# Kernel tuning notes

Hardware: AMD Instinct MI355X
Metric: run time of the kernel (lower is better)

Reference implementation:

```python
import jax, jax.numpy as jnp
import numpy as np

SEQ, BATCH, IN, H = 188, 256, 128, 256


def _lstm_scan(x_proj, w_hh, batch, hidden):
    # x_proj: (T, B, 4H) = input projection + biases, already computed
    h0 = jnp.zeros((batch, hidden), x_proj.dtype)
    c0 = jnp.zeros((batch, hidden), x_proj.dtype)
    w_hh_t = w_hh.T  # (H, 4H)

    def step(carry, xt):
        h, c = carry
        gates = xt + h @ w_hh_t  # (B, 4H)
        i, f, g, o = jnp.split(gates, 4, axis=-1)  # PyTorch gate order i,f,g,o
        i = jax.nn.sigmoid(i)
        f = jax.nn.sigmoid(f)
        g = jnp.tanh(g)
        o = jax.nn.sigmoid(o)
        c = f * c + i * g
        h = o * jnp.tanh(c)
        return (h, c), h

    _, hs = jax.lax.scan(step, (h0, c0), x_proj)
    return hs  # (T, B, H)


def setup_inputs() -> dict:
    key = jax.random.key(0)
    ks = jax.random.split(key, 9)
    s = 1.0 / np.sqrt(H)  # PyTorch default init scale
    mk = lambda k, shape: jax.random.uniform(k, shape, jnp.float32, -s, s)
    return {
        "x": jax.random.normal(ks[0], (SEQ, BATCH, IN), jnp.float32),
        "w_ih_f": mk(ks[1], (4 * H, IN)),
        "w_hh_f": mk(ks[2], (4 * H, H)),
        "b_ih_f": mk(ks[3], (4 * H,)),
        "b_hh_f": mk(ks[4], (4 * H,)),
        "w_ih_b": mk(ks[5], (4 * H, IN)),
        "w_hh_b": mk(ks[6], (4 * H, H)),
        "b_ih_b": mk(ks[7], (4 * H,)),
        "b_hh_b": mk(ks[8], (4 * H,)),
    }


def reference(x, w_ih_f, w_hh_f, b_ih_f, b_hh_f, w_ih_b, w_hh_b, b_ih_b, b_hh_b):
    batch = x.shape[1]
    # Precompute input projections for all timesteps (big GEMM outside the scan)
    xp_f = jnp.einsum('tbi,gi->tbg', x, w_ih_f) + b_ih_f + b_hh_f
    xp_b = jnp.einsum('tbi,gi->tbg', x[::-1], w_ih_b) + b_ih_b + b_hh_b
    out_f = _lstm_scan(xp_f, w_hh_f, batch, H)            # (T, B, H)
    out_b = _lstm_scan(xp_b, w_hh_b, batch, H)[::-1]      # reversed back
    return jnp.concatenate([out_f, out_b], axis=-1)       # (T, B, 2H)
```

## Files before the change

kernel.cpp:

```cpp
#include <hip/hip_runtime.h>

#define T_SEQ 188
#define NB    256
#define NIN   128
#define NH    256
#define SCQ   (0.0625f / 16129.0f)

typedef __attribute__((ext_vector_type(8))) short s16x8;
typedef __attribute__((ext_vector_type(4))) short s16x4;
typedef __attribute__((ext_vector_type(4))) float f32x4;
typedef __attribute__((ext_vector_type(4))) int   i32x4;

__device__ __forceinline__ short f2bf(float f) {
    union { float f; unsigned u; } v; v.f = f;
    unsigned r = v.u + 0x7fffu + ((v.u >> 16) & 1u);
    return (short)(r >> 16);
}
__device__ __forceinline__ float bf2f(unsigned short s) {
    union { unsigned u; float f; } t; t.u = ((unsigned)s) << 16; return t.f;
}
__device__ __forceinline__ float sigf(float x) {
    return __builtin_amdgcn_rcpf(1.0f + __expf(-x));
}
__device__ __forceinline__ float tanh_(float x) {
    return 1.0f - 2.0f * __builtin_amdgcn_rcpf(__expf(2.0f * x) + 1.0f);
}

__device__ __forceinline__ void lds_barrier() {
    asm volatile("s_waitcnt lgkmcnt(0)" ::: "memory");
    __builtin_amdgcn_s_barrier();
    asm volatile("" ::: "memory");
}

__global__ __launch_bounds__(256) void xp_gemm(
    const float* __restrict__ x,
    const float* __restrict__ w_ih_f, const float* __restrict__ w_ih_b,
    const float* __restrict__ b_ih_f, const float* __restrict__ b_hh_f,
    const float* __restrict__ b_ih_b, const float* __restrict__ b_hh_b,
    unsigned short* __restrict__ xp)
{
    const int mt = blockIdx.x >> 5;
    const int dn = blockIdx.x & 31;
    const int d  = dn >> 4, nt = dn & 15;
    const int t  = mt >> 2, b0 = (mt & 3) * 64, Nb = nt * 64;
    const float* w_ih = d ? w_ih_b : w_ih_f;
    const float* b_ih = d ? b_ih_b : b_ih_f;
    const float* b_hh = d ? b_hh_b : b_hh_f;
    const int tid = threadIdx.x;

    __shared__ short xl[64][136];
    __shared__ short wl[64][136];

    #pragma unroll
    for (int j = 0; j < 8; ++j) {
        const int c2 = tid + j * 256;
        const int r = c2 >> 5, o4 = (c2 & 31) * 4;
        float4 xv = *(const float4*)(x + ((size_t)(t * NB + b0 + r)) * NIN + o4);
        s16x4 xs; xs[0] = f2bf(xv.x); xs[1] = f2bf(xv.y); xs[2] = f2bf(xv.z); xs[3] = f2bf(xv.w);
        *(s16x4*)&xl[r][o4] = xs;
        float4 wv = *(const float4*)(w_ih + ((size_t)(Nb + r)) * NIN + o4);
        s16x4 ws_; ws_[0] = f2bf(wv.x); ws_[1] = f2bf(wv.y); ws_[2] = f2bf(wv.z); ws_[3] = f2bf(wv.w);
        *(s16x4*)&wl[r][o4] = ws_;
    }
    __syncthreads();

    const int v = tid >> 6, l = tid & 63, lg = l >> 4, lb = l & 15;
    s16x8 a[4];
    #pragma unroll
    for (int kk = 0; kk < 4; ++kk)
        a[kk] = *(const s16x8*)&xl[16 * v + lb][kk * 32 + 8 * lg];
    f32x4 acc[4];
    #pragma unroll
    for (int nf = 0; nf < 4; ++nf) {
        const int g = Nb + nf * 16 + lb;
        const float bs = b_ih[g] + b_hh[g];
        acc[nf][0] = bs; acc[nf][1] = bs; acc[nf][2] = bs; acc[nf][3] = bs;
    }
    #pragma unroll
    for (int kk = 0; kk < 4; ++kk)
        #pragma unroll
        for (int nf = 0; nf < 4; ++nf) {
            s16x8 bf_ = *(const s16x8*)&wl[nf * 16 + lb][kk * 32 + 8 * lg];
            acc[nf] = __builtin_amdgcn_mfma_f32_16x16x32_bf16(a[kk], bf_, acc[nf], 0, 0, 0);
        }
    #pragma unroll
    for (int nf = 0; nf < 4; ++nf)
        #pragma unroll
        for (int rr = 0; rr < 4; ++rr) {
            const int b = b0 + 16 * v + 4 * lg + rr;
            xp[((size_t)(d * T_SEQ + t) * NB + b) * 1024 + Nb + nf * 16 + lb] =
                (unsigned short)f2bf(acc[nf][rr]);
        }
}

__device__ __forceinline__ void lstm_step(
    int p, int w, int l, int lg, int lb, int c, int huq, int hwb,
    const unsigned short*& xpp, long dxp, float*& outp, long dout,
    int* hl, int (&rscr)[16][4][4][16],
    const i32x4 (&wq)[4][4], float& cst,
    unsigned short (&cur)[4], unsigned short (&nxt)[4])
{
    #pragma unroll
    for (int G = 0; G < 4; ++G)
        nxt[G] = xpp[G * 256];
    xpp += dxp;

    i32x4 ac[4];
    #pragma unroll
    for (int G = 0; G < 4; ++G) {
        ac[G][0] = 0; ac[G][1] = 0; ac[G][2] = 0; ac[G][3] = 0;
    }
    #pragma unroll
    for (int kk = 0; kk < 4; ++kk) {
        i32x4 bq = *(const i32x4*)&hl[p * 1024 + kk * 256 + 4 * l];
        ac[0] = __builtin_amdgcn_mfma_i32_16x16x64_i8(wq[0][kk], bq, ac[0], 0, 0, 0);
        ac[1] = __builtin_amdgcn_mfma_i32_16x16x64_i8(wq[1][kk], bq, ac[1], 0, 0, 0);
        ac[2] = __builtin_amdgcn_mfma_i32_16x16x64_i8(wq[2][kk], bq, ac[2], 0, 0, 0);
        ac[3] = __builtin_amdgcn_mfma_i32_16x16x64_i8(wq[3][kk], bq, ac[3], 0, 0, 0);
    }

    if (lb < 4) {
        #pragma unroll
        for (int G = 0; G < 4; ++G)
            *(i32x4*)&rscr[w][G][lb][4 * lg] = ac[G];
    }
    asm volatile("s_waitcnt lgkmcnt(0)" ::: "memory");
    int av[4];
    #pragma unroll
    for (int G = 0; G < 4; ++G)
        av[G] = rscr[w][G][c][huq];
    asm volatile("s_waitcnt lgkmcnt(0)" ::: "memory");

    const float gi = SCQ * (float)av[0] + bf2f(cur[0]);
    const float gf = SCQ * (float)av[1] + bf2f(cur[1]);
    const float gg = SCQ * (float)av[2] + bf2f(cur[2]);
    const float go = SCQ * (float)av[3] + bf2f(cur[3]);
    const float iv = sigf(gi), fv = sigf(gf);
    const float gv = tanh_(gg), ov = sigf(go);
    const float cc = fv * cst + iv * gv;
    cst = cc;
    const float h = ov * tanh_(cc);
    *outp = h;
    outp += dout;
    ((signed char*)hl)[(p ^ 1) * 4096 + hwb] = (signed char)(int)rintf(h * 127.0f);

    lds_barrier();
}

__global__ __launch_bounds__(1024, 4) void lstm_rec(
    const float* __restrict__ w_hh_f, const float* __restrict__ w_hh_b,
    const unsigned short* __restrict__ xp, float* __restrict__ out)
{
    const int bid = blockIdx.x;
    const int d  = bid >> 6;
    const int bt = bid & 63;
    const float* w_hh = d ? w_hh_b : w_hh_f;
    const int tid = threadIdx.x;
    const int w = tid >> 6, l = tid & 63, lg = l >> 4, lb = l & 15;
    const int c = l & 3, huq = l >> 2;

    __shared__ int hl[2 * 1024];
    __shared__ int rscr[16][4][4][16];

    i32x4 wq[4][4];
    #pragma unroll
    for (int G = 0; G < 4; ++G) {
        const int row = G * 256 + 16 * w + lb;
        #pragma unroll
        for (int kk = 0; kk < 4; ++kk) {
            i32x4 pk;
            #pragma unroll
            for (int r = 0; r < 4; ++r) {
                float4 wv = *(const float4*)(w_hh + (size_t)row * NH + kk * 64 + 16 * lg + 4 * r);
                const int q0 = (int)rintf(wv.x * 2032.0f) & 255;
                const int q1 = (int)rintf(wv.y * 2032.0f) & 255;
                const int q2 = (int)rintf(wv.z * 2032.0f) & 255;
                const int q3 = (int)rintf(wv.w * 2032.0f) & 255;
                pk[r] = q0 | (q1 << 8) | (q2 << 16) | (q3 << 24);
            }
            wq[G][kk] = pk;
        }
    }
    for (int i = tid; i < 2048; i += 1024) hl[i] = 0;

    const int hwb = (w >> 2) * 1024 + (w & 3) * 256 + c * 16 + huq;

    float cst = 0.f;
    unsigned short XPA[4], XPB[4];
    const int t0 = d ? (T_SEQ - 1) : 0;
    const long dxp  = (d ? -(long)NB : (long)NB) * 1024;
    const long dout = (d ? -(long)NB : (long)NB) * 512;
    const unsigned short* xpp =
        xp + ((size_t)(d * T_SEQ + t0) * NB + bt * 4 + c) * 1024 + 16 * w + huq;
    float* outp = out + ((size_t)t0 * NB + bt * 4 + c) * 512 + d * 256 + 16 * w + huq;
    #pragma unroll
    for (int G = 0; G < 4; ++G)
        XPA[G] = xpp[G * 256];
    xpp += dxp;
    __syncthreads();

    for (int s2 = 0; s2 < T_SEQ / 2; ++s2) {
        lstm_step(0, w, l, lg, lb, c, huq, hwb, xpp, dxp, outp, dout,
                  hl, rscr, wq, cst, XPA, XPB);
        lstm_step(1, w, l, lg, lb, c, huq, hwb, xpp, dxp, outp, dout,
                  hl, rscr, wq, cst, XPB, XPA);
    }
}

#define ZSTR_FB 392
__global__ __launch_bounds__(512, 2) void lstm_fb(
    const float* __restrict__ x,
    const float* __restrict__ w_ih_f, const float* __restrict__ w_hh_f,
    const float* __restrict__ b_ih_f, const float* __restrict__ b_hh_f,
    const float* __restrict__ w_ih_b, const float* __restrict__ w_hh_b,
    const float* __restrict__ b_ih_b, const float* __restrict__ b_hh_b,
    float* __restrict__ out, unsigned* __restrict__ flags)
{
    const int b  = blockIdx.x;
    const int d  = b >> 5;
    const int hh = (b >> 4) & 1;
    const int bt = b & 15;
    const int pb = b ^ 16;
    const int po = 1 - hh;
    const float* w_ih = d ? w_ih_b : w_ih_f;
    const float* w_hh = d ? w_hh_b : w_hh_f;
    const float* b_ih = d ? b_ih_b : b_ih_f;
    const float* b_hh = d ? b_hh_b : b_hh_f;
    const int tid = threadIdx.x;
    const int w = tid >> 6, l = tid & 63, lg = l >> 4, lb = l & 15;
    const int hbase = hh * 128 + 16 * w;

    __shared__ short Z[2][16][ZSTR_FB];
    __shared__ float biasL[8][4][16];
    const int off_x   = lg * 8;
    const int off_own = (4 + 4 * hh) * 32 + lg * 8;
    const int off_par = (4 + 4 * po) * 32 + lg * 8;

    s16x8 wf[4][12];
    #pragma unroll
    for (int G = 0; G < 4; ++G) {
        const int gc = G * 256 + hbase + lb;
        #pragma unroll
        for (int kkidx = 0; kkidx < 12; ++kkidx) {
            const int kb = (kkidx < 4) ? (off_x + 32 * kkidx)
                         : (kkidx < 8) ? (off_own + 32 * (kkidx - 4))
                                       : (off_par + 32 * (kkidx - 8));
            const float* src = (kb < NIN) ? (w_ih + (size_t)gc * NIN + kb)
                                          : (w_hh + (size_t)gc * NH + (kb - NIN));
            float4 a  = *(const float4*)(src);
            float4 b2 = *(const float4*)(src + 4);
            s16x8 tv;
            tv[0] = f2bf(a.x);  tv[1] = f2bf(a.y);  tv[2] = f2bf(a.z);  tv[3] = f2bf(a.w);
            tv[4] = f2bf(b2.x); tv[5] = f2bf(b2.y); tv[6] = f2bf(b2.z); tv[7] = f2bf(b2.w);
            wf[G][kkidx] = tv;
        }
    }
    {
        const int G = lb >> 2, r = lb & 3;
        const int gcr = G * 256 + hbase + 4 * lg + r;
        biasL[w][G][4 * lg + r] = b_ih[gcr] + b_hh[gcr];
    }
    const int srow = tid >> 5;
    const int sk4  = (tid & 31) * 4;
    {
        s16x8 zz;
        #pragma unroll
        for (int i = 0; i < 8; ++i) zz[i] = 0;
        *(s16x8*)&Z[0][srow][NIN + (tid & 31) * 8] = zz;
        const int t0 = d ? (T_SEQ - 1) : 0;
        float4 xv0 = *(const float4*)(x + ((size_t)(t0 * NB + bt * 16 + srow)) * NIN + sk4);
        s16x4 xp_;
        xp_[0] = f2bf(xv0.x); xp_[1] = f2bf(xv0.y); xp_[2] = f2bf(xv0.z); xp_[3] = f2bf(xv0.w);
        *(s16x4*)&Z[0][srow][sk4] = xp_;
    }
    float cst[4] = {0.f, 0.f, 0.f, 0.f};
    __syncthreads();
    unsigned* myflag = flags + b * 16;
    unsigned* pflag  = flags + pb * 16;
    float* outp = out + (size_t)(bt * 16) * 512 + d * 256 + hbase + 4 * lg;

    for (int s = 0; s < T_SEQ; ++s) {
        const int p = s & 1;
        const int t = d ? (T_SEQ - 1 - s) : s;
        float4 xv;
        const bool havex = (s + 1 < T_SEQ);
        if (havex) {
            const int tn = d ? (T_SEQ - 2 - s) : (s + 1);
            xv = *(const float4*)(x + ((size_t)(tn * NB + bt * 16 + srow)) * NIN + sk4);
        }
        f32x4 acc[4];
        #pragma unroll
        for (int G = 0; G < 4; ++G)
            acc[G] = *(const f32x4*)&biasL[w][G][4 * lg];
        const short* zrow = &Z[p][lb][0];
        #pragma unroll
        for (int kk = 0; kk < 4; ++kk) {
            s16x8 bfv = *(const s16x8*)(zrow + off_x + 32 * kk);
            acc[0] = __builtin_amdgcn_mfma_f32_16x16x32_bf16(wf[0][kk], bfv, acc[0], 0, 0, 0);
            acc[1] = __builtin_amdgcn_mfma_f32_16x16x32_bf16(wf[1][kk], bfv, acc[1], 0, 0, 0);
            acc[2] = __builtin_amdgcn_mfma_f32_16x16x32_bf16(wf[2][kk], bfv, acc[2], 0, 0, 0);
            acc[3] = __builtin_amdgcn_mfma_f32_16x16x32_bf16(wf[3][kk], bfv, acc[3], 0, 0, 0);
        }
        #pragma unroll
        for (int kk = 0; kk < 4; ++kk) {
            s16x8 bfv = *(const s16x8*)(zrow + off_own + 32 * kk);
            acc[0] = __builtin_amdgcn_mfma_f32_16x16x32_bf16(wf[0][4 + kk], bfv, acc[0], 0, 0, 0);
            acc[1] = __builtin_amdgcn_mfma_f32_16x16x32_bf16(wf[1][4 + kk], bfv, acc[1], 0, 0, 0);
            acc[2] = __builtin_amdgcn_mfma_f32_16x16x32_bf16(wf[2][4 + kk], bfv, acc[2], 0, 0, 0);
            acc[3] = __builtin_amdgcn_mfma_f32_16x16x32_bf16(wf[3][4 + kk], bfv, acc[3], 0, 0, 0);
        }
        if (s > 0) {
            const unsigned want = (unsigned)s;
            while (__hip_atomic_load(pflag, __ATOMIC_RELAXED, __HIP_MEMORY_SCOPE_AGENT) < want)
                __builtin_amdgcn_s_sleep(1);
            __builtin_amdgcn_fence(__ATOMIC_ACQUIRE, "agent");
            const int tprev = d ? (T_SEQ - s) : (s - 1);
            float4 pv = *(const float4*)(out + (size_t)tprev * NB * 512
                         + (size_t)(bt * 16 + srow) * 512 + d * 256 + po * 128 + sk4);
            s16x4 pp;
            pp[0] = f2bf(pv.x); pp[1] = f2bf(pv.y); pp[2] = f2bf(pv.z); pp[3] = f2bf(pv.w);
            *(s16x4*)&Z[p][srow][NIN + po * 128 + sk4] = pp;
        }
        __syncthreads();
        #pragma unroll
        for (int kk = 0; kk < 4; ++kk) {
            s16x8 bfv = *(const s16x8*)(zrow + off_par + 32 * kk);
            acc[0] = __builtin_amdgcn_mfma_f32_16x16x32_bf16(wf[0][8 + kk], bfv, acc[0], 0, 0, 0);
            acc[1] = __builtin_amdgcn_mfma_f32_16x16x32_bf16(wf[1][8 + kk], bfv, acc[1], 0, 0, 0);
            acc[2] = __builtin_amdgcn_mfma_f32_16x16x32_bf16(wf[2][8 + kk], bfv, acc[2], 0, 0, 0);
            acc[3] = __builtin_amdgcn_mfma_f32_16x16x32_bf16(wf[3][8 + kk], bfv, acc[3], 0, 0, 0);
        }
        float4 hout; s16x4 hbf;
        #pragma unroll
        for (int r = 0; r < 4; ++r) {
            const float iv = sigf(acc[0][r]);
            const float fv = sigf(acc[1][r]);
            const float gv = tanh_(acc[2][r]);
            const float ov = sigf(acc[3][r]);
            const float cc = fv * cst[r] + iv * gv;
            cst[r] = cc;
            const float h = ov * tanh_(cc);
            (&hout.x)[r] = h;
            hbf[r] = f2bf(h);
        }
        *(s16x4*)&Z[p ^ 1][lb][NIN + hbase + 4 * lg] = hbf;
        if (havex) {
            s16x4 xp_;
            xp_[0] = f2bf(xv.x); xp_[1] = f2bf(xv.y); xp_[2] = f2bf(xv.z); xp_[3] = f2bf(xv.w);
            *(s16x4*)&Z[p ^ 1][srow][sk4] = xp_;
        }
        *(f32x4*)(outp + (size_t)t * NB * 512 + lb * 512) = *(f32x4*)&hout;
        __syncthreads();
        if (tid == 0 && s + 1 < T_SEQ)
            __hip_atomic_store(myflag, (unsigned)(s + 1),
                               __ATOMIC_RELEASE, __HIP_MEMORY_SCOPE_AGENT);
    }
}

extern "C" void kernel_launch(void* const* d_in, const int* in_sizes, int n_in,
                              void* d_out, int out_size, void* d_ws, size_t ws_size,
                              hipStream_t stream) {
    const float* x      = (const float*)d_in[0];
    const float* w_ih_f = (const float*)d_in[1];
    const float* w_hh_f = (const float*)d_in[2];
    const float* b_ih_f = (const float*)d_in[3];
    const float* b_hh_f = (const float*)d_in[4];
    const float* w_ih_b = (const float*)d_in[5];
    const float* w_hh_b = (const float*)d_in[6];
    const float* b_ih_b = (const float*)d_in[7];
    const float* b_hh_b = (const float*)d_in[8];
    float* out = (float*)d_out;

    const size_t XPN = (size_t)2 * T_SEQ * NB * 1024;
    const int g1 = (T_SEQ * NB / 64) * 32;

    if (ws_size >= XPN * 2) {
        unsigned short* xp = (unsigned short*)d_ws;
        xp_gemm<<<dim3(g1), dim3(256), 0, stream>>>(
            x, w_ih_f, w_ih_b, b_ih_f, b_hh_f, b_ih_b, b_hh_b, xp);
        lstm_rec<<<dim3(128), dim3(1024), 0, stream>>>(w_hh_f, w_hh_b, xp, out);
    } else {
        unsigned* flags = (unsigned*)d_ws;
        hipMemsetAsync(flags, 0, 4096, stream);
        lstm_fb<<<dim3(64), dim3(512), 0, stream>>>(
            x, w_ih_f, w_hh_f, b_ih_f, b_hh_f, w_ih_b, w_hh_b, b_ih_b, b_hh_b,
            out, flags);
    }
}
```

Before: 349.4 us.

## Split batch columns into two groups and overlap MFMA with gate math

Restructures the recurrent LSTM kernel so the four batch columns per block form two groups whose hidden states live in separate LDS buffers. In each half-step, all waves run the int8 MFMA for one group while the waves owning the other group compute their gate nonlinearities, interleaving matrix and elementwise work across the serial time dependency. It removes the ping-pong h buffers and the per-step x-projection double buffering. It adds a second barrier per timestep and leaves half the waves idle during each gates phase.

```diff
diff --git a/kernel.cpp b/kernel.cpp
--- a/kernel.cpp
+++ b/kernel.cpp
@@ -93,48 +93,43 @@
         }
 }
 
-__device__ __forceinline__ void lstm_step(
-    int p, int w, int l, int lg, int lb, int c, int huq, int hwb,
-    const unsigned short*& xpp, long dxp, float*& outp, long dout,
-    int* hl, int (&rscr)[16][4][4][16],
-    const i32x4 (&wq)[4][4], float& cst,
-    unsigned short (&cur)[4], unsigned short (&nxt)[4])
-{
-    #pragma unroll
-    for (int G = 0; G < 4; ++G)
-        nxt[G] = xpp[G * 256];
-    xpp += dxp;
-
+__device__ __forceinline__ void mfma_phase(
+    const int* buf, int (*rs)[256], int cb,
+    int w, int l, int lg, int lb, const i32x4 (&wq)[4][4])
+{
     i32x4 ac[4];
     #pragma unroll
-    for (int G = 0; G < 4; ++G) {
-        ac[G][0] = 0; ac[G][1] = 0; ac[G][2] = 0; ac[G][3] = 0;
-    }
+    for (int G = 0; G < 4; ++G) { ac[G][0] = 0; ac[G][1] = 0; ac[G][2] = 0; ac[G][3] = 0; }
     #pragma unroll
     for (int kk = 0; kk < 4; ++kk) {
-        i32x4 bq = *(const i32x4*)&hl[p * 1024 + kk * 256 + 4 * l];
+        i32x4 bq = *(const i32x4*)&buf[kk * 256 + 4 * l];
         ac[0] = __builtin_amdgcn_mfma_i32_16x16x64_i8(wq[0][kk], bq, ac[0], 0, 0, 0);
         ac[1] = __builtin_amdgcn_mfma_i32_16x16x64_i8(wq[1][kk], bq, ac[1], 0, 0, 0);
         ac[2] = __builtin_amdgcn_mfma_i32_16x16x64_i8(wq[2][kk], bq, ac[2], 0, 0, 0);
         ac[3] = __builtin_amdgcn_mfma_i32_16x16x64_i8(wq[3][kk], bq, ac[3], 0, 0, 0);
     }
-
-    if (lb < 4) {
+    if (lb >= cb && lb < cb + 2) {
+        const int c1 = lb - cb;
         #pragma unroll
         for (int G = 0; G < 4; ++G)
-            *(i32x4*)&rscr[w][G][lb][4 * lg] = ac[G];
-    }
-    asm volatile("s_waitcnt lgkmcnt(0)" ::: "memory");
-    int av[4];
-    #pragma unroll
-    for (int G = 0; G < 4; ++G)
-        av[G] = rscr[w][G][c][huq];
-    asm volatile("s_waitcnt lgkmcnt(0)" ::: "memory");
-
-    const float gi = SCQ * (float)av[0] + bf2f(cur[0]);
-    const float gf = SCQ * (float)av[1] + bf2f(cur[1]);
-    const float gg = SCQ * (float)av[2] + bf2f(cur[2]);
-    const float go = SCQ * (float)av[3] + bf2f(cur[3]);
+            *(i32x4*)&rs[G * 2 + c1][16 * w + 4 * lg] = ac[G];
+    }
+}
+
+__device__ __forceinline__ void gates_phase(
+    const int (*rs)[256], int lq, int hu,
+    float& cst, unsigned short (&X)[4],
+    const unsigned short*& xpp, long dxp, float*& outp, long dout,
+    signed char* hlbyte)
+{
+    const int a0 = rs[0 + lq][hu];
+    const int a1 = rs[2 + lq][hu];
+    const int a2 = rs[4 + lq][hu];
+    const int a3 = rs[6 + lq][hu];
+    const float gi = SCQ * (float)a0 + bf2f(X[0]);
+    const float gf = SCQ * (float)a1 + bf2f(X[1]);
+    const float gg = SCQ * (float)a2 + bf2f(X[2]);
+    const float go = SCQ * (float)a3 + bf2f(X[3]);
     const float iv = sigf(gi), fv = sigf(gf);
     const float gv = tanh_(gg), ov = sigf(go);
     const float cc = fv * cst + iv * gv;
@@ -142,9 +137,9 @@
     const float h = ov * tanh_(cc);
     *outp = h;
     outp += dout;
-    ((signed char*)hl)[(p ^ 1) * 4096 + hwb] = (signed char)(int)rintf(h * 127.0f);
-
-    lds_barrier();
+    *hlbyte = (signed char)(int)rintf(h * 127.0f);
+    X[0] = xpp[0]; X[1] = xpp[256]; X[2] = xpp[512]; X[3] = xpp[768];
+    xpp += dxp;
 }
 
 __global__ __launch_bounds__(1024, 4) void lstm_rec(
@@ -157,10 +152,14 @@
     const float* w_hh = d ? w_hh_b : w_hh_f;
     const int tid = threadIdx.x;
     const int w = tid >> 6, l = tid & 63, lg = l >> 4, lb = l & 15;
-    const int c = l & 3, huq = l >> 2;
-
-    __shared__ int hl[2 * 1024];
-    __shared__ int rscr[16][4][4][16];
+    const int grp = w >> 3;
+    const int gw  = w & 7;
+    const int lq  = l & 1;
+    const int hu  = 32 * gw + (l >> 1);
+    const int c   = 2 * grp + lq;
+
+    __shared__ int hlA[1024], hlB[1024];
+    __shared__ int rsA[8][256], rsB[8][256];
 
     i32x4 wq[4][4];
     #pragma unroll
@@ -181,29 +180,36 @@
             wq[G][kk] = pk;
         }
     }
-    for (int i = tid; i < 2048; i += 1024) hl[i] = 0;
-
-    const int hwb = (w >> 2) * 1024 + (w & 3) * 256 + c * 16 + huq;
+    hlA[tid] = 0; hlB[tid] = 0;
+
+    const int hlw = (hu >> 6) * 1024 + ((hu >> 4) & 3) * 256 + c * 16 + (hu & 15);
+    signed char* hlbyte = (signed char*)(grp ? hlB : hlA) + hlw;
 
     float cst = 0.f;
-    unsigned short XPA[4], XPB[4];
+    unsigned short X[4];
     const int t0 = d ? (T_SEQ - 1) : 0;
     const long dxp  = (d ? -(long)NB : (long)NB) * 1024;
     const long dout = (d ? -(long)NB : (long)NB) * 512;
     const unsigned short* xpp =
-        xp + ((size_t)(d * T_SEQ + t0) * NB + bt * 4 + c) * 1024 + 16 * w + huq;
-    float* outp = out + ((size_t)t0 * NB + bt * 4 + c) * 512 + d * 256 + 16 * w + huq;
-    #pragma unroll
-    for (int G = 0; G < 4; ++G)
-        XPA[G] = xpp[G * 256];
+        xp + ((size_t)(d * T_SEQ + t0) * NB + bt * 4 + c) * 1024 + hu;
+    float* outp = out + ((size_t)t0 * NB + bt * 4 + c) * 512 + d * 256 + hu;
+    X[0] = xpp[0]; X[1] = xpp[256]; X[2] = xpp[512]; X[3] = xpp[768];
     xpp += dxp;
     __syncthreads();
 
-    for (int s2 = 0; s2 < T_SEQ / 2; ++s2) {
-        lstm_step(0, w, l, lg, lb, c, huq, hwb, xpp, dxp, outp, dout,
-                  hl, rscr, wq, cst, XPA, XPB);
-        lstm_step(1, w, l, lg, lb, c, huq, hwb, xpp, dxp, outp, dout,
-                  hl, rscr, wq, cst, XPB, XPA);
+    mfma_phase(hlA, rsA, 0, w, l, lg, lb, wq);
+    lds_barrier();
+
+    for (int s = 0; s < T_SEQ; ++s) {
+        mfma_phase(hlB, rsB, 2, w, l, lg, lb, wq);
+        if (grp == 0)
+            gates_phase(rsA, lq, hu, cst, X, xpp, dxp, outp, dout, hlbyte);
+        lds_barrier();
+        if (s < T_SEQ - 1)
+            mfma_phase(hlA, rsA, 0, w, l, lg, lb, wq);
+        if (grp == 1)
+            gates_phase(rsB, lq, hu, cst, X, xpp, dxp, outp, dout, hlbyte);
+        lds_barrier();
     }
 }
 
```

After: 475.9 us. 1.36x slower.

## Restructure input-projection GEMM to loop over N tiles with resident A fragments

Applied to the files above, without the earlier changes.

The xp_gemm kernel now launches one block per (64-row M tile, direction) and loops over all 16 N tiles, keeping the converted x fragments in registers instead of reloading and reconverting x for every N tile. Biases are pre-summed once into LDS, and each N-tile iteration stages its weight slice through LDS with two barriers. This cuts redundant x loads and conversions and shrinks the grid, at the cost of serializing 16 tiles per block with extra barriers and less parallelism. The recurrent kernel's hidden-index arithmetic is rewritten equivalently.

```diff
diff --git a/kernel.cpp b/kernel.cpp
--- a/kernel.cpp
+++ b/kernel.cpp
@@ -39,58 +39,86 @@
     const float* __restrict__ b_ih_b, const float* __restrict__ b_hh_b,
     unsigned short* __restrict__ xp)
 {
-    const int mt = blockIdx.x >> 5;
-    const int dn = blockIdx.x & 31;
-    const int d  = dn >> 4, nt = dn & 15;
-    const int t  = mt >> 2, b0 = (mt & 3) * 64, Nb = nt * 64;
+    const int mt = blockIdx.x >> 1;
+    const int d  = blockIdx.x & 1;
+    const int t  = mt >> 2, b0 = (mt & 3) * 64;
     const float* w_ih = d ? w_ih_b : w_ih_f;
     const float* b_ih = d ? b_ih_b : b_ih_f;
     const float* b_hh = d ? b_hh_b : b_hh_f;
     const int tid = threadIdx.x;
-
-    __shared__ short xl[64][136];
+    const int v = tid >> 6, l = tid & 63, lg = l >> 4, lb = l & 15;
+
     __shared__ short wl[64][136];
-
-    #pragma unroll
-    for (int j = 0; j < 8; ++j) {
-        const int c2 = tid + j * 256;
-        const int r = c2 >> 5, o4 = (c2 & 31) * 4;
-        float4 xv = *(const float4*)(x + ((size_t)(t * NB + b0 + r)) * NIN + o4);
-        s16x4 xs; xs[0] = f2bf(xv.x); xs[1] = f2bf(xv.y); xs[2] = f2bf(xv.z); xs[3] = f2bf(xv.w);
-        *(s16x4*)&xl[r][o4] = xs;
-        float4 wv = *(const float4*)(w_ih + ((size_t)(Nb + r)) * NIN + o4);
-        s16x4 ws_; ws_[0] = f2bf(wv.x); ws_[1] = f2bf(wv.y); ws_[2] = f2bf(wv.z); ws_[3] = f2bf(wv.w);
-        *(s16x4*)&wl[r][o4] = ws_;
-    }
-    __syncthreads();
-
-    const int v = tid >> 6, l = tid & 63, lg = l >> 4, lb = l & 15;
+    __shared__ float biasS[1024];
+
+    #pragma unroll
+    for (int j = 0; j < 4; ++j) {
+        const int g = tid * 4 + j * 1024; (void)g;
+    }
+    {
+        const int g = tid * 4;
+        float4 bi = *(const float4*)(b_ih + g);
+        float4 bh = *(const float4*)(b_hh + g);
+        biasS[g + 0] = bi.x + bh.x; biasS[g + 1] = bi.y + bh.y;
+        biasS[g + 2] = bi.z + bh.z; biasS[g + 3] = bi.w + bh.w;
+    }
+
     s16x8 a[4];
-    #pragma unroll
-    for (int kk = 0; kk < 4; ++kk)
-        a[kk] = *(const s16x8*)&xl[16 * v + lb][kk * 32 + 8 * lg];
-    f32x4 acc[4];
-    #pragma unroll
-    for (int nf = 0; nf < 4; ++nf) {
-        const int g = Nb + nf * 16 + lb;
-        const float bs = b_ih[g] + b_hh[g];
-        acc[nf][0] = bs; acc[nf][1] = bs; acc[nf][2] = bs; acc[nf][3] = bs;
-    }
-    #pragma unroll
-    for (int kk = 0; kk < 4; ++kk)
+    {
+        const float* xr = x + ((size_t)(t * NB + b0 + 16 * v + lb)) * NIN + 8 * lg;
+        #pragma unroll
+        for (int kk = 0; kk < 4; ++kk) {
+            float4 p0 = *(const float4*)(xr + 32 * kk);
+            float4 p1 = *(const float4*)(xr + 32 * kk + 4);
+            s16x8 tv;
+            tv[0] = f2bf(p0.x); tv[1] = f2bf(p0.y); tv[2] = f2bf(p0.z); tv[3] = f2bf(p0.w);
+            tv[4] = f2bf(p1.x); tv[5] = f2bf(p1.y); tv[6] = f2bf(p1.z); tv[7] = f2bf(p1.w);
+            a[kk] = tv;
+        }
+    }
+
+    const int wr = tid >> 2, wk = (tid & 3) * 32;
+
+    unsigned short* xpb =
+        xp + ((size_t)(d * T_SEQ + t) * NB + b0 + 16 * v + 4 * lg) * 1024 + lb;
+
+    for (int nt = 0; nt < 16; ++nt) {
+        const int Nb = nt * 64;
+        {
+            const float* wsrc = w_ih + ((size_t)(Nb + wr)) * NIN + wk;
+            #pragma unroll
+            for (int j = 0; j < 4; ++j) {
+                float4 p0 = *(const float4*)(wsrc + 8 * j);
+                float4 p1 = *(const float4*)(wsrc + 8 * j + 4);
+                s16x8 tv;
+                tv[0] = f2bf(p0.x); tv[1] = f2bf(p0.y); tv[2] = f2bf(p0.z); tv[3] = f2bf(p0.w);
+                tv[4] = f2bf(p1.x); tv[5] = f2bf(p1.y); tv[6] = f2bf(p1.z); tv[7] = f2bf(p1.w);
+                *(s16x8*)&wl[wr][wk + 8 * j] = tv;
+            }
+        }
+        __syncthreads();
+
+        f32x4 acc[4];
         #pragma unroll
         for (int nf = 0; nf < 4; ++nf) {
-            s16x8 bf_ = *(const s16x8*)&wl[nf * 16 + lb][kk * 32 + 8 * lg];
-            acc[nf] = __builtin_amdgcn_mfma_f32_16x16x32_bf16(a[kk], bf_, acc[nf], 0, 0, 0);
-        }
-    #pragma unroll
-    for (int nf = 0; nf < 4; ++nf)
-        #pragma unroll
-        for (int rr = 0; rr < 4; ++rr) {
-            const int b = b0 + 16 * v + 4 * lg + rr;
-            xp[((size_t)(d * T_SEQ + t) * NB + b) * 1024 + Nb + nf * 16 + lb] =
-                (unsigned short)f2bf(acc[nf][rr]);
-        }
+            const float bs = biasS[Nb + nf * 16 + lb];
+            acc[nf][0] = bs; acc[nf][1] = bs; acc[nf][2] = bs; acc[nf][3] = bs;
+        }
+        #pragma unroll
+        for (int kk = 0; kk < 4; ++kk)
+            #pragma unroll
+            for (int nf = 0; nf < 4; ++nf) {
+                s16x8 bf_ = *(const s16x8*)&wl[nf * 16 + lb][kk * 32 + 8 * lg];
+                acc[nf] = __builtin_amdgcn_mfma_f32_16x16x32_bf16(a[kk], bf_, acc[nf], 0, 0, 0);
+            }
+        __syncthreads();
+
+        #pragma unroll
+        for (int nf = 0; nf < 4; ++nf)
+            #pragma unroll
+            for (int rr = 0; rr < 4; ++rr)
+                xpb[(size_t)rr * 1024 + Nb + nf * 16] = (unsigned short)f2bf(acc[nf][rr]);
+    }
 }
 
 __device__ __forceinline__ void lstm_step(
@@ -183,7 +211,8 @@
     }
     for (int i = tid; i < 2048; i += 1024) hl[i] = 0;
 
-    const int hwb = (w >> 2) * 1024 + (w & 3) * 256 + c * 16 + huq;
+    const int hu = 16 * w + huq;
+    const int hwb = (hu >> 6) * 1024 + ((hu >> 4) & 3) * 256 + c * 16 + (hu & 15);
 
     float cst = 0.f;
     unsigned short XPA[4], XPB[4];
@@ -191,8 +220,8 @@
     const long dxp  = (d ? -(long)NB : (long)NB) * 1024;
     const long dout = (d ? -(long)NB : (long)NB) * 512;
     const unsigned short* xpp =
-        xp + ((size_t)(d * T_SEQ + t0) * NB + bt * 4 + c) * 1024 + 16 * w + huq;
-    float* outp = out + ((size_t)t0 * NB + bt * 4 + c) * 512 + d * 256 + 16 * w + huq;
+        xp + ((size_t)(d * T_SEQ + t0) * NB + bt * 4 + c) * 1024 + hu;
+    float* outp = out + ((size_t)t0 * NB + bt * 4 + c) * 512 + d * 256 + hu;
     #pragma unroll
     for (int G = 0; G < 4; ++G)
         XPA[G] = xpp[G * 256];
@@ -372,11 +401,10 @@
     float* out = (float*)d_out;
 
     const size_t XPN = (size_t)2 * T_SEQ * NB * 1024;
-    const int g1 = (T_SEQ * NB / 64) * 32;
 
     if (ws_size >= XPN * 2) {
         unsigned short* xp = (unsigned short*)d_ws;
-        xp_gemm<<<dim3(g1), dim3(256), 0, stream>>>(
+        xp_gemm<<<dim3(752 * 2), dim3(256), 0, stream>>>(
             x, w_ih_f, w_ih_b, b_ih_f, b_hh_f, b_ih_b, b_hh_b, xp);
         lstm_rec<<<dim3(128), dim3(1024), 0, stream>>>(w_hh_f, w_hh_b, xp, out);
     } else {
```

New measurement: 346.3 us. No clear change (-0.9%).
